# Kernel optimization log

Measured on AMD Instinct MI355X. Metric: run time of the kernel, lower is better.

The kernel has to match this reference:

```python
import jax, jax.numpy as jnp
import numpy as np

B, SQ, SV, D = 4, 4096, 4096, 64


def setup_inputs() -> dict:
    key = jax.random.key(0)
    kq, kv = jax.random.split(key)
    query = jax.random.normal(kq, (B, SQ, D), dtype=jnp.float32)
    value = jax.random.normal(kv, (B, SV, D), dtype=jnp.float32)
    return {"query": query, "value": value}


def reference(query, value):
    # scores: [B, Sq, Sv] = Q @ V^T  (no scale, no mask, as in the original)
    scores = jnp.einsum("bqd,bvd->bqv", query, value)
    weights = jax.nn.softmax(scores, axis=-1)
    # output: [B, Sq, D]
    return jnp.einsum("bqv,bvd->bqd", weights, value)
```

## Files before the change

kernel.cpp:

```cpp
#include <hip/hip_runtime.h>
#include <hip/hip_bf16.h>
#include <stdint.h>

#define BATCH 4
#define SQN   4096
#define SVN   4096
#define DIM   64
#define KT    32
#define NTILE (SVN / KT)
#define NSTEP 32

#define RMS 72
#define TRS 40
#define IMG_RM_H 0
#define IMG_RM_L 4608
#define IMG_TR_H 9216
#define IMG_TR_L 14336
#define BLOB     19456
#define NCHUNK   19
#define LDS_BYTES (8 * BLOB)

typedef __attribute__((ext_vector_type(8))) short bf16x8;
typedef __attribute__((ext_vector_type(4))) float f32x4;
typedef __attribute__((ext_vector_type(4))) unsigned int u32x4;

#if __has_builtin(__builtin_amdgcn_exp2f)
#define EXP2F __builtin_amdgcn_exp2f
#else
#define EXP2F exp2f
#endif

static __device__ __forceinline__ unsigned short bf16_rne(float x) {
  unsigned u = __float_as_uint(x);
  u += 0x7FFFu + ((u >> 16) & 1u);
  return (unsigned short)(u >> 16);
}
static __device__ __forceinline__ float bf16f(unsigned short h) {
  return __uint_as_float((unsigned)h << 16);
}
static __device__ __forceinline__ unsigned cvt_pk_bf16(float lo, float hi) {
  unsigned r;
  asm("v_cvt_pk_bf16_f32 %0, %1, %2" : "=v"(r) : "v"(lo), "v"(hi));
  return r;
}

__global__ __launch_bounds__(256) void vprep_kernel(const float* __restrict__ V,
                                                    char* __restrict__ ws) {
  __shared__ __align__(16) char sbuf[BLOB];
  const int b    = blockIdx.x >> 7;
  const int tile = blockIdx.x & 127;
  const int t    = threadIdx.x;
  const int vv   = t >> 3;
  const int d0   = (t & 7) * 8;

  const float* src = V + (((size_t)b * SVN + (size_t)tile * KT + vv) * DIM + d0);
  const float4 a0 = ((const float4*)src)[0];
  const float4 a1 = ((const float4*)src)[1];
  const float x[8] = {a0.x, a0.y, a0.z, a0.w, a1.x, a1.y, a1.z, a1.w};

  unsigned short h[8], l[8];
#pragma unroll
  for (int j = 0; j < 8; ++j) {
    h[j] = bf16_rne(x[j]);
    l[j] = bf16_rne(x[j] - bf16f(h[j]));
  }

  const int p = (((vv >> 2) & 1) << 4) | ((vv >> 3) << 2) | (vv & 3);
  bf16x8 vh, vl;
#pragma unroll
  for (int j = 0; j < 8; ++j) { vh[j] = (short)h[j]; vl[j] = (short)l[j]; }
  *(bf16x8*)(sbuf + IMG_RM_H + (p * RMS + d0) * 2) = vh;
  *(bf16x8*)(sbuf + IMG_RM_L + (p * RMS + d0) * 2) = vl;

  unsigned short* trh = (unsigned short*)(sbuf + IMG_TR_H);
  unsigned short* trl = (unsigned short*)(sbuf + IMG_TR_L);
#pragma unroll
  for (int j = 0; j < 8; ++j) {
    trh[(d0 + j) * TRS + vv] = h[j];
    trl[(d0 + j) * TRS + vv] = l[j];
  }
  __syncthreads();

  float4* dst = (float4*)(ws + (size_t)(b * NTILE + tile) * BLOB);
  const float4* s4 = (const float4*)sbuf;
#pragma unroll
  for (int k = 0; k < 5; ++k) {
    const int idx = t + k * 256;
    if (idx < BLOB / 16) dst[idx] = s4[idx];
  }
}

__global__ __launch_bounds__(512, 2) void attn_kernel(const float* __restrict__ Qg,
                                                      const char* __restrict__ vprep,
                                                      float* __restrict__ out) {
  extern __shared__ char smem[];
  const int raw = blockIdx.x;
  const int lb = (raw & 7) * 32 + (raw >> 3);
  const int batch = lb >> 6;
  const int qbase = (lb & 63) * 64;
  const int tid = threadIdx.x;
  const int lane = tid & 63;
  const int wid = tid >> 6;
  const int qt = wid & 1;
  const int quarter = wid >> 1;
  const int lr = lane & 15;
  const int lg = lane >> 4;

  bf16x8 Qh[2][2], Ql[2][2];
#pragma unroll
  for (int qb = 0; qb < 2; ++qb) {
    const size_t qrow = (size_t)batch * SQN + qbase + qt * 32 + qb * 16 + lr;
#pragma unroll
    for (int ks = 0; ks < 2; ++ks) {
      const float* qp = Qg + qrow * DIM + ks * 32 + 8 * lg;
      const float4 f0 = ((const float4*)qp)[0];
      const float4 f1 = ((const float4*)qp)[1];
      const float xv[8] = {f0.x, f0.y, f0.z, f0.w, f1.x, f1.y, f1.z, f1.w};
#pragma unroll
      for (int j = 0; j < 8; ++j) {
        const float v = xv[j] * 1.44269504088896f;
        const unsigned short hh = bf16_rne(v);
        Qh[qb][ks][j] = (short)hh;
        Ql[qb][ks][j] = (short)bf16_rne(v - bf16f(hh));
      }
    }
  }

  f32x4 Oacc[2][4];
#pragma unroll
  for (int qb = 0; qb < 2; ++qb)
#pragma unroll
    for (int db = 0; db < 4; ++db) Oacc[qb][db] = (f32x4){0.f, 0.f, 0.f, 0.f};
  float m_[2] = {-1e30f, -1e30f};
  float l_[2] = {0.f, 0.f};

  const size_t tb0 = (size_t)(batch * NTILE) * BLOB;
  const int sq = wid >> 1;
  const int sh = wid & 1;

  auto stage = [&](int t, int b) {
#pragma unroll
    for (int k = 0; k < 10; ++k) {
      const int sub = sh + 2 * k;
      if (sub < NCHUNK) {
        const char* g = vprep + tb0 + (size_t)(sq * NSTEP + t) * BLOB + sub * 1024 + lane * 16;
        char* lp = smem + (sq * 2 + b) * BLOB + sub * 1024;
        __builtin_amdgcn_global_load_lds(
            (const __attribute__((address_space(1))) unsigned int*)g,
            (__attribute__((address_space(3))) unsigned int*)lp, 16, 0, 0);
      }
    }
  };

  stage(0, 0);
  __syncthreads();
  int buf = 0;

  for (int t = 0; t < NSTEP; ++t) {
    if (t + 1 < NSTEP) stage(t + 1, buf ^ 1);

    const char* qbuf = smem + (quarter * 2 + buf) * BLOB;

    bf16x8 Vh[2][2], Vl[2][2];
#pragma unroll
    for (int vt = 0; vt < 2; ++vt)
#pragma unroll
      for (int ks = 0; ks < 2; ++ks) {
        const int off = ((vt * 16 + lr) * RMS + ks * 32 + 8 * lg) * 2;
        Vh[vt][ks] = *(const bf16x8*)(qbuf + IMG_RM_H + off);
        Vl[vt][ks] = *(const bf16x8*)(qbuf + IMG_RM_L + off);
      }

    f32x4 sacc[2][2];
#pragma unroll
    for (int qb = 0; qb < 2; ++qb)
#pragma unroll
      for (int vt = 0; vt < 2; ++vt) {
        f32x4 acc = (f32x4){0.f, 0.f, 0.f, 0.f};
#pragma unroll
        for (int ks = 0; ks < 2; ++ks) {
          acc = __builtin_amdgcn_mfma_f32_16x16x32_bf16(Vh[vt][ks], Qh[qb][ks], acc, 0, 0, 0);
          acc = __builtin_amdgcn_mfma_f32_16x16x32_bf16(Vh[vt][ks], Ql[qb][ks], acc, 0, 0, 0);
          acc = __builtin_amdgcn_mfma_f32_16x16x32_bf16(Vl[vt][ks], Qh[qb][ks], acc, 0, 0, 0);
        }
        sacc[qb][vt] = acc;
      }

    bf16x8 Ph[2], Pl[2];
#pragma unroll
    for (int qb = 0; qb < 2; ++qb) {
      float mt = -1e30f;
#pragma unroll
      for (int vt = 0; vt < 2; ++vt)
#pragma unroll
        for (int r = 0; r < 4; ++r) mt = fmaxf(mt, sacc[qb][vt][r]);
      mt = fmaxf(mt, __shfl_xor(mt, 16, 64));
      mt = fmaxf(mt, __shfl_xor(mt, 32, 64));
      const float mnew = fmaxf(m_[qb], mt);
      const float alpha = EXP2F(m_[qb] - mnew);
      float p[8];
      float rs = 0.f;
#pragma unroll
      for (int vt = 0; vt < 2; ++vt)
#pragma unroll
        for (int r = 0; r < 4; ++r) {
          const float pv = EXP2F(sacc[qb][vt][r] - mnew);
          p[vt * 4 + r] = pv;
          rs += pv;
        }
      rs += __shfl_xor(rs, 16, 64);
      rs += __shfl_xor(rs, 32, 64);
      l_[qb] = l_[qb] * alpha + rs;
      m_[qb] = mnew;
#pragma unroll
      for (int db = 0; db < 4; ++db) Oacc[qb][db] *= alpha;
      u32x4 hu, lu;
#pragma unroll
      for (int j = 0; j < 4; ++j) {
        const unsigned hd = cvt_pk_bf16(p[2 * j], p[2 * j + 1]);
        const float h0 = __uint_as_float(hd << 16);
        const float h1 = __uint_as_float(hd & 0xFFFF0000u);
        hu[j] = hd;
        lu[j] = cvt_pk_bf16(p[2 * j] - h0, p[2 * j + 1] - h1);
      }
      Ph[qb] = __builtin_bit_cast(bf16x8, hu);
      Pl[qb] = __builtin_bit_cast(bf16x8, lu);
    }

#pragma unroll
    for (int db = 0; db < 4; ++db) {
      const int toff = ((db * 16 + lr) * TRS + 8 * lg) * 2;
      const bf16x8 Ah = *(const bf16x8*)(qbuf + IMG_TR_H + toff);
      const bf16x8 Al = *(const bf16x8*)(qbuf + IMG_TR_L + toff);
#pragma unroll
      for (int qb = 0; qb < 2; ++qb) {
        Oacc[qb][db] = __builtin_amdgcn_mfma_f32_16x16x32_bf16(Ah, Ph[qb], Oacc[qb][db], 0, 0, 0);
        Oacc[qb][db] = __builtin_amdgcn_mfma_f32_16x16x32_bf16(Al, Ph[qb], Oacc[qb][db], 0, 0, 0);
        Oacc[qb][db] = __builtin_amdgcn_mfma_f32_16x16x32_bf16(Ah, Pl[qb], Oacc[qb][db], 0, 0, 0);
      }
    }

    __syncthreads();
    buf ^= 1;
  }

  float* mbuf = (float*)smem;
  float* mlb  = (float*)(smem + 2 * 4 * 32 * 68 * 4);
#pragma unroll
  for (int qb = 0; qb < 2; ++qb) {
    const int q = qb * 16 + lr;
    float* dst = mbuf + ((qt * 4 + quarter) * 32 + q) * 68;
#pragma unroll
    for (int db = 0; db < 4; ++db)
#pragma unroll
      for (int r = 0; r < 4; ++r) dst[db * 16 + 4 * lg + r] = Oacc[qb][db][r];
  }
  if (lg == 0) {
#pragma unroll
    for (int qb = 0; qb < 2; ++qb) {
      const int q = qb * 16 + lr;
      mlb[((qt * 4 + quarter) * 32 + q) * 2 + 0] = m_[qb];
      mlb[((qt * 4 + quarter) * 32 + q) * 2 + 1] = l_[qb];
    }
  }
  __syncthreads();

  const int q_all = tid >> 3;
  const int d0 = (tid & 7) * 8;
  const int qt2 = q_all >> 5;
  const int qq = q_all & 31;
  float M = -1e30f;
#pragma unroll
  for (int w = 0; w < 4; ++w) M = fmaxf(M, mlb[((qt2 * 4 + w) * 32 + qq) * 2]);
  float L = 0.f;
  float o[8] = {0, 0, 0, 0, 0, 0, 0, 0};
#pragma unroll
  for (int w = 0; w < 4; ++w) {
    const float a = EXP2F(mlb[((qt2 * 4 + w) * 32 + qq) * 2] - M);
    L += a * mlb[((qt2 * 4 + w) * 32 + qq) * 2 + 1];
    const float* srcp = mbuf + ((qt2 * 4 + w) * 32 + qq) * 68 + d0;
#pragma unroll
    for (int j = 0; j < 8; ++j) o[j] += a * srcp[j];
  }
  const float inv = 1.0f / L;
  float* op = out + ((size_t)batch * SQN + qbase + qt2 * 32 + qq) * DIM + d0;
  float4 w0 = {o[0] * inv, o[1] * inv, o[2] * inv, o[3] * inv};
  float4 w1 = {o[4] * inv, o[5] * inv, o[6] * inv, o[7] * inv};
  ((float4*)op)[0] = w0;
  ((float4*)op)[1] = w1;
}

extern "C" void kernel_launch(void* const* d_in, const int* in_sizes, int n_in,
                              void* d_out, int out_size, void* d_ws, size_t ws_size,
                              hipStream_t stream) {
  const float* Qg = (const float*)d_in[0];
  const float* Vg = (const float*)d_in[1];
  float* out = (float*)d_out;
  char* ws = (char*)d_ws;
  const size_t need = (size_t)BATCH * NTILE * BLOB;
  if (ws_size < need) return;

  hipFuncSetAttribute((const void*)attn_kernel,
                      hipFuncAttributeMaxDynamicSharedMemorySize, LDS_BYTES);

  vprep_kernel<<<BATCH * NTILE, 256, 0, stream>>>(Vg, ws);
  attn_kernel<<<256, 512, LDS_BYTES, stream>>>(Qg, ws, out);
}
```

Baseline: 134.4 us.

## Split attention into smaller blocks with lazy rescale, priority hints, and direct vprep writes

The attention kernel now uses 256-thread blocks covering 32 queries, with the key sequence split across two halves instead of four quarters, and the grid doubled to 512 blocks. Each wave now processes one 16-query tile, and LDS per block is halved. The online softmax skips the rescale unless the running max grows by more than a threshold. The loop also adds s_setprio around the MFMA sections and uses an explicit vmcnt wait plus barrier at the top of the loop. The V-prep kernel writes the row-major image straight to global memory and builds the transposed image through a packed LDS exchange. These changes trade reuse of V tiles across queries (each staged tile now serves fewer queries) for more blocks, less LDS, and less softmax work per step.

```diff
diff --git a/kernel.cpp b/kernel.cpp
--- a/kernel.cpp
+++ b/kernel.cpp
@@ -8,7 +8,7 @@
 #define DIM   64
 #define KT    32
 #define NTILE (SVN / KT)
-#define NSTEP 32
+#define NSTEPH 64
 
 #define RMS 72
 #define TRS 40
@@ -17,8 +17,7 @@
 #define IMG_TR_H 9216
 #define IMG_TR_L 14336
 #define BLOB     19456
-#define NCHUNK   19
-#define LDS_BYTES (8 * BLOB)
+#define LDS_BYTES (4 * BLOB)
 
 typedef __attribute__((ext_vector_type(8))) short bf16x8;
 typedef __attribute__((ext_vector_type(4))) float f32x4;
@@ -46,7 +45,7 @@
 
 __global__ __launch_bounds__(256) void vprep_kernel(const float* __restrict__ V,
                                                     char* __restrict__ ws) {
-  __shared__ __align__(16) char sbuf[BLOB];
+  __shared__ unsigned ex[32][65];
   const int b    = blockIdx.x >> 7;
   const int tile = blockIdx.x & 127;
   const int t    = threadIdx.x;
@@ -65,51 +64,58 @@
     l[j] = bf16_rne(x[j] - bf16f(h[j]));
   }
 
+  char* blob = ws + (size_t)(b * NTILE + tile) * BLOB;
+
   const int p = (((vv >> 2) & 1) << 4) | ((vv >> 3) << 2) | (vv & 3);
   bf16x8 vh, vl;
 #pragma unroll
   for (int j = 0; j < 8; ++j) { vh[j] = (short)h[j]; vl[j] = (short)l[j]; }
-  *(bf16x8*)(sbuf + IMG_RM_H + (p * RMS + d0) * 2) = vh;
-  *(bf16x8*)(sbuf + IMG_RM_L + (p * RMS + d0) * 2) = vl;
-
-  unsigned short* trh = (unsigned short*)(sbuf + IMG_TR_H);
-  unsigned short* trl = (unsigned short*)(sbuf + IMG_TR_L);
-#pragma unroll
-  for (int j = 0; j < 8; ++j) {
-    trh[(d0 + j) * TRS + vv] = h[j];
-    trl[(d0 + j) * TRS + vv] = l[j];
-  }
+  *(bf16x8*)(blob + IMG_RM_H + (p * RMS + d0) * 2) = vh;
+  *(bf16x8*)(blob + IMG_RM_L + (p * RMS + d0) * 2) = vl;
+
+#pragma unroll
+  for (int j = 0; j < 8; ++j) ex[vv][d0 + j] = (unsigned)h[j] | ((unsigned)l[j] << 16);
   __syncthreads();
 
-  float4* dst = (float4*)(ws + (size_t)(b * NTILE + tile) * BLOB);
-  const float4* s4 = (const float4*)sbuf;
-#pragma unroll
-  for (int k = 0; k < 5; ++k) {
-    const int idx = t + k * 256;
-    if (idx < BLOB / 16) dst[idx] = s4[idx];
-  }
-}
-
-__global__ __launch_bounds__(512, 2) void attn_kernel(const float* __restrict__ Qg,
+  const int r  = t >> 1;
+  const int pl = r >> 6;
+  const int d  = r & 63;
+  const int hh = t & 1;
+  unsigned w16[16];
+#pragma unroll
+  for (int c = 0; c < 16; ++c) w16[c] = ex[hh * 16 + c][d];
+  u32x4 o0, o1;
+#pragma unroll
+  for (int k = 0; k < 8; ++k) {
+    const unsigned w0 = w16[2 * k], w1 = w16[2 * k + 1];
+    const unsigned dw = pl ? ((w0 >> 16) | (w1 & 0xFFFF0000u))
+                           : ((w0 & 0xFFFFu) | (w1 << 16));
+    if (k < 4) o0[k] = dw; else o1[k - 4] = dw;
+  }
+  char* dst = blob + (pl ? IMG_TR_L : IMG_TR_H) + (d * TRS + hh * 16) * 2;
+  ((u32x4*)dst)[0] = o0;
+  ((u32x4*)dst)[1] = o1;
+}
+
+__global__ __launch_bounds__(256, 2) void attn_kernel(const float* __restrict__ Qg,
                                                       const char* __restrict__ vprep,
                                                       float* __restrict__ out) {
   extern __shared__ char smem[];
   const int raw = blockIdx.x;
-  const int lb = (raw & 7) * 32 + (raw >> 3);
-  const int batch = lb >> 6;
-  const int qbase = (lb & 63) * 64;
+  const int lb = (raw & 7) * 64 + (raw >> 3);
+  const int batch = lb >> 7;
+  const int qbase = (lb & 127) * 32;
   const int tid = threadIdx.x;
   const int lane = tid & 63;
   const int wid = tid >> 6;
   const int qt = wid & 1;
-  const int quarter = wid >> 1;
+  const int half = wid >> 1;
   const int lr = lane & 15;
   const int lg = lane >> 4;
 
-  bf16x8 Qh[2][2], Ql[2][2];
-#pragma unroll
-  for (int qb = 0; qb < 2; ++qb) {
-    const size_t qrow = (size_t)batch * SQN + qbase + qt * 32 + qb * 16 + lr;
+  bf16x8 Qh[2], Ql[2];
+  {
+    const size_t qrow = (size_t)batch * SQN + qbase + qt * 16 + lr;
 #pragma unroll
     for (int ks = 0; ks < 2; ++ks) {
       const float* qp = Qg + qrow * DIM + ks * 32 + 8 * lg;
@@ -120,46 +126,42 @@
       for (int j = 0; j < 8; ++j) {
         const float v = xv[j] * 1.44269504088896f;
         const unsigned short hh = bf16_rne(v);
-        Qh[qb][ks][j] = (short)hh;
-        Ql[qb][ks][j] = (short)bf16_rne(v - bf16f(hh));
-      }
-    }
-  }
-
-  f32x4 Oacc[2][4];
-#pragma unroll
-  for (int qb = 0; qb < 2; ++qb)
-#pragma unroll
-    for (int db = 0; db < 4; ++db) Oacc[qb][db] = (f32x4){0.f, 0.f, 0.f, 0.f};
-  float m_[2] = {-1e30f, -1e30f};
-  float l_[2] = {0.f, 0.f};
+        Qh[ks][j] = (short)hh;
+        Ql[ks][j] = (short)bf16_rne(v - bf16f(hh));
+      }
+    }
+  }
+
+  f32x4 Oacc[4];
+#pragma unroll
+  for (int db = 0; db < 4; ++db) Oacc[db] = (f32x4){0.f, 0.f, 0.f, 0.f};
+  float m_ = -1e30f;
+  float l_ = 0.f;
 
   const size_t tb0 = (size_t)(batch * NTILE) * BLOB;
-  const int sq = wid >> 1;
-  const int sh = wid & 1;
 
   auto stage = [&](int t, int b) {
+    const size_t g0 = tb0 + (size_t)(half * NSTEPH + t) * BLOB;
+    char* l0 = smem + (half * 2 + b) * BLOB;
+    const int c0 = qt * 9;
 #pragma unroll
     for (int k = 0; k < 10; ++k) {
-      const int sub = sh + 2 * k;
-      if (sub < NCHUNK) {
-        const char* g = vprep + tb0 + (size_t)(sq * NSTEP + t) * BLOB + sub * 1024 + lane * 16;
-        char* lp = smem + (sq * 2 + b) * BLOB + sub * 1024;
-        __builtin_amdgcn_global_load_lds(
-            (const __attribute__((address_space(1))) unsigned int*)g,
-            (__attribute__((address_space(3))) unsigned int*)lp, 16, 0, 0);
-      }
+      const int sub = c0 + k;
+      __builtin_amdgcn_global_load_lds(
+          (const __attribute__((address_space(1))) unsigned int*)(vprep + g0 + sub * 1024 + lane * 16),
+          (__attribute__((address_space(3))) unsigned int*)(l0 + sub * 1024), 16, 0, 0);
     }
   };
 
   stage(0, 0);
-  __syncthreads();
   int buf = 0;
 
-  for (int t = 0; t < NSTEP; ++t) {
-    if (t + 1 < NSTEP) stage(t + 1, buf ^ 1);
-
-    const char* qbuf = smem + (quarter * 2 + buf) * BLOB;
+  for (int t = 0; t < NSTEPH; ++t) {
+    asm volatile("s_waitcnt vmcnt(0)" ::: "memory");
+    __builtin_amdgcn_s_barrier();
+    if (t + 1 < NSTEPH) stage(t + 1, buf ^ 1);
+
+    const char* qbuf = smem + (half * 2 + buf) * BLOB;
 
     bf16x8 Vh[2][2], Vl[2][2];
 #pragma unroll
@@ -171,49 +173,64 @@
         Vl[vt][ks] = *(const bf16x8*)(qbuf + IMG_RM_L + off);
       }
 
-    f32x4 sacc[2][2];
-#pragma unroll
-    for (int qb = 0; qb < 2; ++qb)
-#pragma unroll
-      for (int vt = 0; vt < 2; ++vt) {
-        f32x4 acc = (f32x4){0.f, 0.f, 0.f, 0.f};
-#pragma unroll
-        for (int ks = 0; ks < 2; ++ks) {
-          acc = __builtin_amdgcn_mfma_f32_16x16x32_bf16(Vh[vt][ks], Qh[qb][ks], acc, 0, 0, 0);
-          acc = __builtin_amdgcn_mfma_f32_16x16x32_bf16(Vh[vt][ks], Ql[qb][ks], acc, 0, 0, 0);
-          acc = __builtin_amdgcn_mfma_f32_16x16x32_bf16(Vl[vt][ks], Qh[qb][ks], acc, 0, 0, 0);
-        }
-        sacc[qb][vt] = acc;
-      }
-
-    bf16x8 Ph[2], Pl[2];
-#pragma unroll
-    for (int qb = 0; qb < 2; ++qb) {
+    f32x4 sacc[2];
+    __builtin_amdgcn_s_setprio(1);
+#pragma unroll
+    for (int vt = 0; vt < 2; ++vt) {
+      f32x4 acc = (f32x4){0.f, 0.f, 0.f, 0.f};
+#pragma unroll
+      for (int ks = 0; ks < 2; ++ks) {
+        acc = __builtin_amdgcn_mfma_f32_16x16x32_bf16(Vh[vt][ks], Qh[ks], acc, 0, 0, 0);
+        acc = __builtin_amdgcn_mfma_f32_16x16x32_bf16(Vh[vt][ks], Ql[ks], acc, 0, 0, 0);
+        acc = __builtin_amdgcn_mfma_f32_16x16x32_bf16(Vl[vt][ks], Qh[ks], acc, 0, 0, 0);
+      }
+      sacc[vt] = acc;
+    }
+    __builtin_amdgcn_s_setprio(0);
+
+    bf16x8 Ph, Pl;
+    {
       float mt = -1e30f;
 #pragma unroll
       for (int vt = 0; vt < 2; ++vt)
 #pragma unroll
-        for (int r = 0; r < 4; ++r) mt = fmaxf(mt, sacc[qb][vt][r]);
+        for (int r = 0; r < 4; ++r) mt = fmaxf(mt, sacc[vt][r]);
       mt = fmaxf(mt, __shfl_xor(mt, 16, 64));
       mt = fmaxf(mt, __shfl_xor(mt, 32, 64));
-      const float mnew = fmaxf(m_[qb], mt);
-      const float alpha = EXP2F(m_[qb] - mnew);
+
       float p[8];
       float rs = 0.f;
-#pragma unroll
-      for (int vt = 0; vt < 2; ++vt)
-#pragma unroll
-        for (int r = 0; r < 4; ++r) {
-          const float pv = EXP2F(sacc[qb][vt][r] - mnew);
-          p[vt * 4 + r] = pv;
-          rs += pv;
-        }
-      rs += __shfl_xor(rs, 16, 64);
-      rs += __shfl_xor(rs, 32, 64);
-      l_[qb] = l_[qb] * alpha + rs;
-      m_[qb] = mnew;
-#pragma unroll
-      for (int db = 0; db < 4; ++db) Oacc[qb][db] *= alpha;
+      if (__any(mt > m_ + 8.0f)) {
+        const float mnew = fmaxf(m_, mt);
+        const float alpha = EXP2F(m_ - mnew);
+#pragma unroll
+        for (int vt = 0; vt < 2; ++vt)
+#pragma unroll
+          for (int r = 0; r < 4; ++r) {
+            const float pv = EXP2F(sacc[vt][r] - mnew);
+            p[vt * 4 + r] = pv;
+            rs += pv;
+          }
+        rs += __shfl_xor(rs, 16, 64);
+        rs += __shfl_xor(rs, 32, 64);
+        l_ = l_ * alpha + rs;
+        m_ = mnew;
+#pragma unroll
+        for (int db = 0; db < 4; ++db) Oacc[db] *= alpha;
+      } else {
+#pragma unroll
+        for (int vt = 0; vt < 2; ++vt)
+#pragma unroll
+          for (int r = 0; r < 4; ++r) {
+            const float pv = EXP2F(sacc[vt][r] - m_);
+            p[vt * 4 + r] = pv;
+            rs += pv;
+          }
+        rs += __shfl_xor(rs, 16, 64);
+        rs += __shfl_xor(rs, 32, 64);
+        l_ += rs;
+      }
+
       u32x4 hu, lu;
 #pragma unroll
       for (int j = 0; j < 4; ++j) {
@@ -223,67 +240,59 @@
         hu[j] = hd;
         lu[j] = cvt_pk_bf16(p[2 * j] - h0, p[2 * j + 1] - h1);
       }
-      Ph[qb] = __builtin_bit_cast(bf16x8, hu);
-      Pl[qb] = __builtin_bit_cast(bf16x8, lu);
-    }
-
+      Ph = __builtin_bit_cast(bf16x8, hu);
+      Pl = __builtin_bit_cast(bf16x8, lu);
+    }
+
+    __builtin_amdgcn_s_setprio(1);
 #pragma unroll
     for (int db = 0; db < 4; ++db) {
       const int toff = ((db * 16 + lr) * TRS + 8 * lg) * 2;
       const bf16x8 Ah = *(const bf16x8*)(qbuf + IMG_TR_H + toff);
       const bf16x8 Al = *(const bf16x8*)(qbuf + IMG_TR_L + toff);
-#pragma unroll
-      for (int qb = 0; qb < 2; ++qb) {
-        Oacc[qb][db] = __builtin_amdgcn_mfma_f32_16x16x32_bf16(Ah, Ph[qb], Oacc[qb][db], 0, 0, 0);
-        Oacc[qb][db] = __builtin_amdgcn_mfma_f32_16x16x32_bf16(Al, Ph[qb], Oacc[qb][db], 0, 0, 0);
-        Oacc[qb][db] = __builtin_amdgcn_mfma_f32_16x16x32_bf16(Ah, Pl[qb], Oacc[qb][db], 0, 0, 0);
-      }
-    }
-
-    __syncthreads();
+      Oacc[db] = __builtin_amdgcn_mfma_f32_16x16x32_bf16(Ah, Ph, Oacc[db], 0, 0, 0);
+      Oacc[db] = __builtin_amdgcn_mfma_f32_16x16x32_bf16(Al, Ph, Oacc[db], 0, 0, 0);
+      Oacc[db] = __builtin_amdgcn_mfma_f32_16x16x32_bf16(Ah, Pl, Oacc[db], 0, 0, 0);
+    }
+    __builtin_amdgcn_s_setprio(0);
+
     buf ^= 1;
   }
 
+  __syncthreads();
+
   float* mbuf = (float*)smem;
-  float* mlb  = (float*)(smem + 2 * 4 * 32 * 68 * 4);
-#pragma unroll
-  for (int qb = 0; qb < 2; ++qb) {
-    const int q = qb * 16 + lr;
-    float* dst = mbuf + ((qt * 4 + quarter) * 32 + q) * 68;
+  float* mlb  = (float*)(smem + 2 * 32 * 68 * 4);
+  {
+    const int ridx = half * 32 + qt * 16 + lr;
+    float* dst = mbuf + ridx * 68;
 #pragma unroll
     for (int db = 0; db < 4; ++db)
 #pragma unroll
-      for (int r = 0; r < 4; ++r) dst[db * 16 + 4 * lg + r] = Oacc[qb][db][r];
-  }
-  if (lg == 0) {
-#pragma unroll
-    for (int qb = 0; qb < 2; ++qb) {
-      const int q = qb * 16 + lr;
-      mlb[((qt * 4 + quarter) * 32 + q) * 2 + 0] = m_[qb];
-      mlb[((qt * 4 + quarter) * 32 + q) * 2 + 1] = l_[qb];
+      for (int r = 0; r < 4; ++r) dst[db * 16 + 4 * lg + r] = Oacc[db][r];
+    if (lg == 0) {
+      mlb[ridx * 2 + 0] = m_;
+      mlb[ridx * 2 + 1] = l_;
     }
   }
   __syncthreads();
 
-  const int q_all = tid >> 3;
+  const int q  = tid >> 3;
   const int d0 = (tid & 7) * 8;
-  const int qt2 = q_all >> 5;
-  const int qq = q_all & 31;
-  float M = -1e30f;
-#pragma unroll
-  for (int w = 0; w < 4; ++w) M = fmaxf(M, mlb[((qt2 * 4 + w) * 32 + qq) * 2]);
+  float M = fmaxf(mlb[q * 2], mlb[(32 + q) * 2]);
   float L = 0.f;
   float o[8] = {0, 0, 0, 0, 0, 0, 0, 0};
 #pragma unroll
-  for (int w = 0; w < 4; ++w) {
-    const float a = EXP2F(mlb[((qt2 * 4 + w) * 32 + qq) * 2] - M);
-    L += a * mlb[((qt2 * 4 + w) * 32 + qq) * 2 + 1];
-    const float* srcp = mbuf + ((qt2 * 4 + w) * 32 + qq) * 68 + d0;
+  for (int hf = 0; hf < 2; ++hf) {
+    const int ridx = hf * 32 + q;
+    const float a = EXP2F(mlb[ridx * 2] - M);
+    L += a * mlb[ridx * 2 + 1];
+    const float* srcp = mbuf + ridx * 68 + d0;
 #pragma unroll
     for (int j = 0; j < 8; ++j) o[j] += a * srcp[j];
   }
   const float inv = 1.0f / L;
-  float* op = out + ((size_t)batch * SQN + qbase + qt2 * 32 + qq) * DIM + d0;
+  float* op = out + ((size_t)batch * SQN + qbase + q) * DIM + d0;
   float4 w0 = {o[0] * inv, o[1] * inv, o[2] * inv, o[3] * inv};
   float4 w1 = {o[4] * inv, o[5] * inv, o[6] * inv, o[7] * inv};
   ((float4*)op)[0] = w0;
@@ -304,5 +313,5 @@
                       hipFuncAttributeMaxDynamicSharedMemorySize, LDS_BYTES);
 
   vprep_kernel<<<BATCH * NTILE, 256, 0, stream>>>(Vg, ws);
-  attn_kernel<<<256, 512, LDS_BYTES, stream>>>(Qg, ws, out);
-}
+  attn_kernel<<<512, 256, LDS_BYTES, stream>>>(Qg, ws, out);
+}
```

New measurement: 153.8 us. 14.4% more time.
